# Optimization experiments

Hardware: AMD Instinct MI355X
Metric: run time of the kernel (lower is better)

## Reference

```python
import jax, jax.numpy as jnp
import numpy as np

N = 100000   # nodes
E = 3200000  # edges (avg degree 32)
G = 512      # graphs in batch
IN = 128     # in_channels
H1, C1 = 8, 8  # conv1 heads, per-head channels
OUT = 64     # out_channels (conv2, 1 head)
NEG_SLOPE = 0.2


def setup_inputs() -> dict:
    key = jax.random.key(0)
    ks = jax.random.split(key, 12)
    s = 0.1
    return dict(
        x=jax.random.normal(ks[0], (N, IN), jnp.float32),
        edge_index=jax.random.randint(ks[1], (2, E), 0, N),
        batch=jnp.sort(jax.random.randint(ks[2], (N,), 0, G)),
        W1=jax.random.normal(ks[3], (IN, H1 * C1), jnp.float32) * s,
        att_src1=jax.random.normal(ks[4], (H1, C1), jnp.float32) * s,
        att_dst1=jax.random.normal(ks[5], (H1, C1), jnp.float32) * s,
        b1=jnp.zeros((H1 * C1,), jnp.float32),
        W2=jax.random.normal(ks[6], (H1 * C1, OUT), jnp.float32) * s,
        att_src2=jax.random.normal(ks[7], (1, OUT), jnp.float32) * s,
        att_dst2=jax.random.normal(ks[8], (1, OUT), jnp.float32) * s,
        b2=jnp.zeros((OUT,), jnp.float32),
        lw1=jax.random.normal(ks[9], (OUT, 128), jnp.float32) * s,
        lb1=jnp.zeros((128,), jnp.float32),
        lw2=jax.random.normal(ks[10], (128, 1), jnp.float32) * s,
        lb2=jnp.zeros((1,), jnp.float32),
    )


def gat_layer(x, src, dst, W, a_src, a_dst, bias, heads, outc):
    # PyG GATConv (eval mode): linear -> per-edge leaky_relu attention ->
    # segment softmax over incoming edges per dst -> weighted scatter-add.
    n = x.shape[0]
    h = (x @ W).reshape(n, heads, outc)                      # [N,H,C]
    a_s = jnp.einsum('nhc,hc->nh', h, a_src)                 # [N,H]
    a_d = jnp.einsum('nhc,hc->nh', h, a_dst)
    e = jax.nn.leaky_relu(a_s[src] + a_d[dst], NEG_SLOPE)    # [E',H]
    m = jax.ops.segment_max(e, dst, num_segments=n)
    m = jax.lax.stop_gradient(jnp.where(jnp.isfinite(m), m, 0.0))
    ex = jnp.exp(e - m[dst])
    denom = jax.ops.segment_sum(ex, dst, num_segments=n)
    alpha = ex / jnp.maximum(denom[dst], 1e-16)              # [E',H]
    out = jax.ops.segment_sum(h[src] * alpha[:, :, None], dst, num_segments=n)
    return out.reshape(n, heads * outc) + bias


def reference(x, W1, att_src1, att_dst1, b1, W2, att_src2, att_dst2, b2,
              lw1, lb1, lw2, lb2, edge_index, batch):
    n = x.shape[0]
    loops = jnp.arange(n)                                    # add_self_loops=True
    src = jnp.concatenate([edge_index[0], loops])
    dst = jnp.concatenate([edge_index[1], loops])
    h = jax.nn.elu(gat_layer(x, src, dst, W1, att_src1, att_dst1, b1, H1, C1))
    h = gat_layer(h, src, dst, W2, att_src2, att_dst2, b2, 1, OUT)  # [N,OUT]
    # global_mean_pool
    s = jax.ops.segment_sum(h, batch, num_segments=G)
    cnt = jax.ops.segment_sum(jnp.ones((n, 1), h.dtype), batch, num_segments=G)
    g = s / jnp.maximum(cnt, 1.0)                            # [G,OUT]
    g = jax.nn.elu(g @ lw1 + lb1)
    return g @ lw2 + lb2                                     # [G,1]
```

## Files before the change

### kernel.cpp

```cpp
#include <hip/hip_runtime.h>
#include <hip/hip_fp16.h>
#include <math.h>

#define NN   100000
#define EE   3200000
#define GG   512
#define INC  128
#define D1   64
#define OUTC 64
#define HID  128
#define NEG  0.2f

#define BINS 391
#define BCAP 9216
#define BKBLK 1563

typedef __attribute__((ext_vector_type(2))) float v2f;

__global__ __launch_bounds__(256)
void k_fused(const int* __restrict__ srcv, const int* __restrict__ dstv,
             int* __restrict__ cursor, int* __restrict__ bucket,
             const float* __restrict__ x, const float* __restrict__ W1,
             const float* __restrict__ att_s, const float* __restrict__ att_d,
             unsigned int* __restrict__ h1, __half* __restrict__ a_s,
             float* __restrict__ a_d) {
    __shared__ __align__(16) char smem[45824];
    int tid = threadIdx.x;
    if (blockIdx.x < BKBLK) {
        int* hcnt  = (int*)smem;
        int* hbase = hcnt + BINS;
        for (int i = tid; i < BINS; i += 256) hcnt[i] = 0;
        __syncthreads();
        int e0 = blockIdx.x * 2048;
        int bn[8], rk[8], pk[8];
#pragma unroll
        for (int q = 0; q < 8; ++q) {
            int e = e0 + q * 256 + tid;
            if (e < EE) {
                int s = srcv[e], d = dstv[e];
                bn[q] = d >> 8;
                pk[q] = (s << 8) | (d & 255);
                rk[q] = atomicAdd(&hcnt[bn[q]], 1);
            } else bn[q] = -1;
        }
        __syncthreads();
        for (int i = tid; i < BINS; i += 256) {
            int c = hcnt[i];
            hbase[i] = c ? atomicAdd(&cursor[i], c) : 0;
        }
        __syncthreads();
#pragma unroll
        for (int q = 0; q < 8; ++q) {
            if (bn[q] >= 0) {
                int p = hbase[bn[q]] + rk[q];
                if (p < BCAP) bucket[bn[q] * BCAP + p] = pk[q];
            }
        }
    } else {
        float4* sW4 = (float4*)smem;
        float (*sx)[INC + 4] = (float(*)[INC + 4])(smem + 32768);
        float (*sh)[D1] = (float(*)[D1])(smem + 32768 + 8448);
        float* satt = (float*)(smem + 32768 + 8448 + 4096);
        const float4* W4 = (const float4*)W1;
        for (int i = tid; i < INC * 16; i += 256) sW4[i] = W4[i];
        if (tid < 128) satt[tid] = (tid < 64) ? att_s[tid] : att_d[tid - 64];
        int node0 = (blockIdx.x - BKBLK) * 16;
        for (int i = tid; i < 16 * 32; i += 256) {
            int r = i >> 5, kk = i & 31;
            float4 v = ((const float4*)x)[(node0 + r) * 32 + kk];
            sx[r][kk * 4 + 0] = v.x; sx[r][kk * 4 + 1] = v.y;
            sx[r][kk * 4 + 2] = v.z; sx[r][kk * 4 + 3] = v.w;
        }
        __syncthreads();
        int r = tid >> 4, cg = tid & 15;
        float4 acc = {0.f, 0.f, 0.f, 0.f};
#pragma unroll 8
        for (int k = 0; k < INC; ++k) {
            float xv = sx[r][k];
            float4 wv = sW4[k * 16 + cg];
            acc.x = fmaf(xv, wv.x, acc.x);
            acc.y = fmaf(xv, wv.y, acc.y);
            acc.z = fmaf(xv, wv.z, acc.z);
            acc.w = fmaf(xv, wv.w, acc.w);
        }
        int p = __builtin_amdgcn_cvt_pk_fp8_f32(acc.x, acc.y, 0, false);
        p = __builtin_amdgcn_cvt_pk_fp8_f32(acc.z, acc.w, p, true);
        h1[(node0 + r) * 16 + cg] = (unsigned int)p;
        sh[r][cg * 4 + 0] = acc.x; sh[r][cg * 4 + 1] = acc.y;
        sh[r][cg * 4 + 2] = acc.z; sh[r][cg * 4 + 3] = acc.w;
        __syncthreads();
        if (tid < 128) {
            int rr = tid >> 3, hh = tid & 7;
            float as = 0.f, ad = 0.f;
#pragma unroll
            for (int j = 0; j < 8; ++j) {
                float v = sh[rr][hh * 8 + j];
                as = fmaf(v, satt[hh * 8 + j], as);
                ad = fmaf(v, satt[64 + hh * 8 + j], ad);
            }
            int nb = node0 + rr;
            a_s[nb * 8 + hh] = __float2half(as);
            a_d[nb * 8 + hh] = ad;
        }
    }
}

__global__ __launch_bounds__(256)
void k_binCSR(const int* __restrict__ cursor, const int* __restrict__ bucket,
              int* __restrict__ col, int* __restrict__ rbeg, int* __restrict__ rend) {
    __shared__ int cnt[256];
    __shared__ int tmp[256];
    __shared__ int cur[256];
    int b = blockIdx.x, tid = threadIdx.x;
    cnt[tid] = 0;
    __syncthreads();
    int m = cursor[b]; if (m > BCAP) m = BCAP;
    const int* seg = bucket + b * BCAP;
    for (int i = tid; i < m; i += 256)
        atomicAdd(&cnt[seg[i] & 255], 1);
    __syncthreads();
    tmp[tid] = cnt[tid];
    __syncthreads();
    for (int off = 1; off < 256; off <<= 1) {
        int t = (tid >= off) ? tmp[tid - off] : 0;
        __syncthreads();
        tmp[tid] += t;
        __syncthreads();
    }
    int excl = tmp[tid] - cnt[tid];
    int n = b * 256 + tid;
    if (n < NN) {
        rbeg[n] = b * BCAP + excl;
        rend[n] = b * BCAP + excl + cnt[tid];
    }
    cur[tid] = excl;
    __syncthreads();
    for (int i = tid; i < m; i += 256) {
        int pkv = seg[i];
        int r = atomicAdd(&cur[pkv & 255], 1);
        col[b * BCAP + r] = pkv >> 8;
    }
}

__global__ __launch_bounds__(256, 8)
void k_gat_agg1(const int* __restrict__ rbeg, const int* __restrict__ rend,
                const int* __restrict__ col,
                const __half* __restrict__ a_s, const float* __restrict__ a_d,
                const unsigned int* __restrict__ h1, const float* __restrict__ b1,
                float* __restrict__ out) {
    int wv = threadIdx.x >> 6;
    int lane = threadIdx.x & 63;
    int half = lane >> 5;
    int d = blockIdx.x * 8 + wv * 2 + half;
    int gs = (lane >> 3) & 3;
    int l = lane & 7;
    int rb = rbeg[d], re = rend[d];
    float adh = a_d[d * 8 + l];
    const uint2* hp = (const uint2*)h1;
    uint2 rself = hp[d * 8 + l];
    float asself = __half2float(a_s[d * 8 + l]);
    float ac[8] = {0.f,0.f,0.f,0.f,0.f,0.f,0.f,0.f};
    float denom = 0.f;
    int e = rb + gs;
    int s[4];
#pragma unroll
    for (int q = 0; q < 4; ++q) s[q] = col[e + 4 * q];
    for (; e + 12 < re; ) {
        uint2 rr[4]; float asv[4]; int sn[4];
#pragma unroll
        for (int q = 0; q < 4; ++q) rr[q] = hp[s[q] * 8 + l];
#pragma unroll
        for (int q = 0; q < 4; ++q) asv[q] = __half2float(a_s[s[q] * 8 + l]);
        int en = e + 16;
#pragma unroll
        for (int q = 0; q < 4; ++q) sn[q] = col[en + 4 * q];
#pragma unroll
        for (int q = 0; q < 4; ++q) {
            float xx = asv[q] + adh;
            xx = xx >= 0.f ? xx : NEG * xx;
            float w = __expf(xx);
            denom += w;
            v2f f0 = __builtin_amdgcn_cvt_pk_f32_fp8((int)rr[q].x, false);
            v2f f1 = __builtin_amdgcn_cvt_pk_f32_fp8((int)rr[q].x, true);
            v2f f2 = __builtin_amdgcn_cvt_pk_f32_fp8((int)rr[q].y, false);
            v2f f3 = __builtin_amdgcn_cvt_pk_f32_fp8((int)rr[q].y, true);
            ac[0] = fmaf(f0.x, w, ac[0]); ac[1] = fmaf(f0.y, w, ac[1]);
            ac[2] = fmaf(f1.x, w, ac[2]); ac[3] = fmaf(f1.y, w, ac[3]);
            ac[4] = fmaf(f2.x, w, ac[4]); ac[5] = fmaf(f2.y, w, ac[5]);
            ac[6] = fmaf(f3.x, w, ac[6]); ac[7] = fmaf(f3.y, w, ac[7]);
        }
        e = en;
#pragma unroll
        for (int q = 0; q < 4; ++q) s[q] = sn[q];
    }
    for (; e < re; e += 4) {
        int s0 = col[e];
        uint2 r0 = hp[s0 * 8 + l];
        float x0 = __half2float(a_s[s0 * 8 + l]) + adh;
        x0 = x0 >= 0.f ? x0 : NEG * x0;
        float w0 = __expf(x0);
        denom += w0;
        v2f f0 = __builtin_amdgcn_cvt_pk_f32_fp8((int)r0.x, false);
        v2f f1 = __builtin_amdgcn_cvt_pk_f32_fp8((int)r0.x, true);
        v2f f2 = __builtin_amdgcn_cvt_pk_f32_fp8((int)r0.y, false);
        v2f f3 = __builtin_amdgcn_cvt_pk_f32_fp8((int)r0.y, true);
        ac[0] = fmaf(f0.x, w0, ac[0]); ac[1] = fmaf(f0.y, w0, ac[1]);
        ac[2] = fmaf(f1.x, w0, ac[2]); ac[3] = fmaf(f1.y, w0, ac[3]);
        ac[4] = fmaf(f2.x, w0, ac[4]); ac[5] = fmaf(f2.y, w0, ac[5]);
        ac[6] = fmaf(f3.x, w0, ac[6]); ac[7] = fmaf(f3.y, w0, ac[7]);
    }
    if (gs == 0) {
        float es = asself + adh;
        es = es >= 0.f ? es : NEG * es;
        float w = __expf(es);
        denom += w;
        v2f f0 = __builtin_amdgcn_cvt_pk_f32_fp8((int)rself.x, false);
        v2f f1 = __builtin_amdgcn_cvt_pk_f32_fp8((int)rself.x, true);
        v2f f2 = __builtin_amdgcn_cvt_pk_f32_fp8((int)rself.y, false);
        v2f f3 = __builtin_amdgcn_cvt_pk_f32_fp8((int)rself.y, true);
        ac[0] = fmaf(f0.x, w, ac[0]); ac[1] = fmaf(f0.y, w, ac[1]);
        ac[2] = fmaf(f1.x, w, ac[2]); ac[3] = fmaf(f1.y, w, ac[3]);
        ac[4] = fmaf(f2.x, w, ac[4]); ac[5] = fmaf(f2.y, w, ac[5]);
        ac[6] = fmaf(f3.x, w, ac[6]); ac[7] = fmaf(f3.y, w, ac[7]);
    }
#pragma unroll
    for (int i = 0; i < 8; ++i) {
        ac[i] += __shfl_xor(ac[i], 8, 64);
        ac[i] += __shfl_xor(ac[i], 16, 64);
    }
    denom += __shfl_xor(denom, 8, 64);
    denom += __shfl_xor(denom, 16, 64);
    if (gs == 0) {
        float inv = 1.0f / denom;
        float4 b0 = ((const float4*)b1)[l * 2];
        float4 b4 = ((const float4*)b1)[l * 2 + 1];
        float4 r0, r1;
        r0.x = fmaf(ac[0], inv, b0.x); r0.x = r0.x > 0.f ? r0.x : expm1f(r0.x);
        r0.y = fmaf(ac[1], inv, b0.y); r0.y = r0.y > 0.f ? r0.y : expm1f(r0.y);
        r0.z = fmaf(ac[2], inv, b0.z); r0.z = r0.z > 0.f ? r0.z : expm1f(r0.z);
        r0.w = fmaf(ac[3], inv, b0.w); r0.w = r0.w > 0.f ? r0.w : expm1f(r0.w);
        r1.x = fmaf(ac[4], inv, b4.x); r1.x = r1.x > 0.f ? r1.x : expm1f(r1.x);
        r1.y = fmaf(ac[5], inv, b4.y); r1.y = r1.y > 0.f ? r1.y : expm1f(r1.y);
        r1.z = fmaf(ac[6], inv, b4.z); r1.z = r1.z > 0.f ? r1.z : expm1f(r1.z);
        r1.w = fmaf(ac[7], inv, b4.w); r1.w = r1.w > 0.f ? r1.w : expm1f(r1.w);
        ((float4*)out)[d * 16 + l * 2]     = r0;
        ((float4*)out)[d * 16 + l * 2 + 1] = r1;
    }
}

__global__ __launch_bounds__(256)
void k_lin2(const float* __restrict__ hin, const float* __restrict__ W2,
            const float* __restrict__ att_s, const float* __restrict__ att_d,
            unsigned int* __restrict__ h2, float* __restrict__ a_s,
            float* __restrict__ a_d) {
    __shared__ float4 sW4[D1 * 16];
    __shared__ float sx[16][D1 + 4];
    __shared__ float satt[2 * OUTC];
    int tid = threadIdx.x;
    const float4* W4 = (const float4*)W2;
    for (int i = tid; i < D1 * 16; i += 256) sW4[i] = W4[i];
    if (tid < 128) satt[tid] = (tid < 64) ? att_s[tid] : att_d[tid - 64];
    int node0 = blockIdx.x * 16;
    for (int i = tid; i < 16 * 16; i += 256) {
        int r = i >> 4, kk = i & 15;
        float4 v = ((const float4*)hin)[(node0 + r) * 16 + kk];
        sx[r][kk * 4 + 0] = v.x; sx[r][kk * 4 + 1] = v.y;
        sx[r][kk * 4 + 2] = v.z; sx[r][kk * 4 + 3] = v.w;
    }
    __syncthreads();
    int r = tid >> 4, cg = tid & 15;
    float4 acc = {0.f, 0.f, 0.f, 0.f};
#pragma unroll 8
    for (int k = 0; k < D1; ++k) {
        float xv = sx[r][k];
        float4 wv = sW4[k * 16 + cg];
        acc.x = fmaf(xv, wv.x, acc.x);
        acc.y = fmaf(xv, wv.y, acc.y);
        acc.z = fmaf(xv, wv.z, acc.z);
        acc.w = fmaf(xv, wv.w, acc.w);
    }
    int n = node0 + r;
    int p = __builtin_amdgcn_cvt_pk_fp8_f32(acc.x, acc.y, 0, false);
    p = __builtin_amdgcn_cvt_pk_fp8_f32(acc.z, acc.w, p, true);
    h2[n * 16 + cg] = (unsigned int)p;
    float vs = acc.x * satt[cg * 4] + acc.y * satt[cg * 4 + 1]
             + acc.z * satt[cg * 4 + 2] + acc.w * satt[cg * 4 + 3];
    float vd = acc.x * satt[64 + cg * 4] + acc.y * satt[64 + cg * 4 + 1]
             + acc.z * satt[64 + cg * 4 + 2] + acc.w * satt[64 + cg * 4 + 3];
    for (int off = 1; off < 16; off <<= 1) {
        vs += __shfl_xor(vs, off, 64);
        vd += __shfl_xor(vd, off, 64);
    }
    if (cg == 0) { a_s[n] = vs; a_d[n] = vd; }
}

__global__ __launch_bounds__(256, 8)
void k_gat_agg2(const int* __restrict__ rbeg, const int* __restrict__ rend,
                const int* __restrict__ col,
                const float* __restrict__ a_s, const float* __restrict__ a_d,
                const unsigned int* __restrict__ h2, const float* __restrict__ b2,
                const int* __restrict__ batch,
                float* __restrict__ pool, float* __restrict__ cnt) {
    __shared__ float sv[8][64];
    __shared__ int sgi[8];
    int wv = threadIdx.x >> 6;
    int lane = threadIdx.x & 63;
    int half = lane >> 5;
    int idx = wv * 2 + half;
    int d = blockIdx.x * 8 + idx;
    int gs = (lane >> 3) & 3;
    int l = lane & 7;
    int rb = rbeg[d], re = rend[d];
    float ad = a_d[d];
    const uint2* hp = (const uint2*)h2;
    uint2 rself = hp[d * 8 + l];
    float asself = a_s[d];
    if (gs == 0 && l == 0) sgi[idx] = batch[d];
    float ac[8] = {0.f,0.f,0.f,0.f,0.f,0.f,0.f,0.f};
    float denom = 0.f;
    int e = rb + gs;
    int s[4];
#pragma unroll
    for (int q = 0; q < 4; ++q) s[q] = col[e + 4 * q];
    for (; e + 12 < re; ) {
        uint2 rr[4]; float asv[4]; int sn[4];
#pragma unroll
        for (int q = 0; q < 4; ++q) rr[q] = hp[s[q] * 8 + l];
#pragma unroll
        for (int q = 0; q < 4; ++q) asv[q] = a_s[s[q]];
        int en = e + 16;
#pragma unroll
        for (int q = 0; q < 4; ++q) sn[q] = col[en + 4 * q];
#pragma unroll
        for (int q = 0; q < 4; ++q) {
            float xx = asv[q] + ad;
            xx = xx >= 0.f ? xx : NEG * xx;
            float w = __expf(xx);
            denom += w;
            v2f f0 = __builtin_amdgcn_cvt_pk_f32_fp8((int)rr[q].x, false);
            v2f f1 = __builtin_amdgcn_cvt_pk_f32_fp8((int)rr[q].x, true);
            v2f f2 = __builtin_amdgcn_cvt_pk_f32_fp8((int)rr[q].y, false);
            v2f f3 = __builtin_amdgcn_cvt_pk_f32_fp8((int)rr[q].y, true);
            ac[0] = fmaf(f0.x, w, ac[0]); ac[1] = fmaf(f0.y, w, ac[1]);
            ac[2] = fmaf(f1.x, w, ac[2]); ac[3] = fmaf(f1.y, w, ac[3]);
            ac[4] = fmaf(f2.x, w, ac[4]); ac[5] = fmaf(f2.y, w, ac[5]);
            ac[6] = fmaf(f3.x, w, ac[6]); ac[7] = fmaf(f3.y, w, ac[7]);
        }
        e = en;
#pragma unroll
        for (int q = 0; q < 4; ++q) s[q] = sn[q];
    }
    for (; e < re; e += 4) {
        int s0 = col[e];
        uint2 r0 = hp[s0 * 8 + l];
        float x0 = a_s[s0] + ad;
        x0 = x0 >= 0.f ? x0 : NEG * x0;
        float w0 = __expf(x0);
        denom += w0;
        v2f f0 = __builtin_amdgcn_cvt_pk_f32_fp8((int)r0.x, false);
        v2f f1 = __builtin_amdgcn_cvt_pk_f32_fp8((int)r0.x, true);
        v2f f2 = __builtin_amdgcn_cvt_pk_f32_fp8((int)r0.y, false);
        v2f f3 = __builtin_amdgcn_cvt_pk_f32_fp8((int)r0.y, true);
        ac[0] = fmaf(f0.x, w0, ac[0]); ac[1] = fmaf(f0.y, w0, ac[1]);
        ac[2] = fmaf(f1.x, w0, ac[2]); ac[3] = fmaf(f1.y, w0, ac[3]);
        ac[4] = fmaf(f2.x, w0, ac[4]); ac[5] = fmaf(f2.y, w0, ac[5]);
        ac[6] = fmaf(f3.x, w0, ac[6]); ac[7] = fmaf(f3.y, w0, ac[7]);
    }
    if (gs == 0) {
        float es = asself + ad;
        es = es >= 0.f ? es : NEG * es;
        float w = __expf(es);
        denom += w;
        v2f f0 = __builtin_amdgcn_cvt_pk_f32_fp8((int)rself.x, false);
        v2f f1 = __builtin_amdgcn_cvt_pk_f32_fp8((int)rself.x, true);
        v2f f2 = __builtin_amdgcn_cvt_pk_f32_fp8((int)rself.y, false);
        v2f f3 = __builtin_amdgcn_cvt_pk_f32_fp8((int)rself.y, true);
        ac[0] = fmaf(f0.x, w, ac[0]); ac[1] = fmaf(f0.y, w, ac[1]);
        ac[2] = fmaf(f1.x, w, ac[2]); ac[3] = fmaf(f1.y, w, ac[3]);
        ac[4] = fmaf(f2.x, w, ac[4]); ac[5] = fmaf(f2.y, w, ac[5]);
        ac[6] = fmaf(f3.x, w, ac[6]); ac[7] = fmaf(f3.y, w, ac[7]);
    }
#pragma unroll
    for (int i = 0; i < 8; ++i) {
        ac[i] += __shfl_xor(ac[i], 8, 64);
        ac[i] += __shfl_xor(ac[i], 16, 64);
    }
    denom += __shfl_xor(denom, 8, 64);
    denom += __shfl_xor(denom, 16, 64);
    if (gs == 0) {
        float inv = 1.0f / denom;
#pragma unroll
        for (int i = 0; i < 8; ++i)
            sv[idx][l * 8 + i] = fmaf(ac[i], inv, b2[l * 8 + i]);
    }
    __syncthreads();
    int tid = threadIdx.x;
    if (tid < 64) {
        float acc = sv[0][tid]; int curg = sgi[0];
        for (int r = 1; r < 8; ++r) {
            if (sgi[r] == curg) acc += sv[r][tid];
            else { atomicAdd(&pool[curg * 64 + tid], acc); curg = sgi[r]; acc = sv[r][tid]; }
        }
        atomicAdd(&pool[curg * 64 + tid], acc);
    } else if (tid == 64) {
        float c = 1.f; int curg = sgi[0];
        for (int r = 1; r < 8; ++r) {
            if (sgi[r] == curg) c += 1.f;
            else { atomicAdd(&cnt[curg], c); curg = sgi[r]; c = 1.f; }
        }
        atomicAdd(&cnt[curg], c);
    }
}

__global__ __launch_bounds__(128)
void k_mlp(const float* __restrict__ pool, const float* __restrict__ cnt,
           const float* __restrict__ lw1, const float* __restrict__ lb1,
           const float* __restrict__ lw2, const float* __restrict__ lb2,
           float* __restrict__ out) {
    __shared__ float sg[OUTC];
    __shared__ float sh[HID];
    int g = blockIdx.x, tid = threadIdx.x;
    float c = fmaxf(cnt[g], 1.0f);
    if (tid < OUTC) sg[tid] = pool[g * OUTC + tid] / c;
    __syncthreads();
    float acc = lb1[tid];
#pragma unroll 8
    for (int k = 0; k < OUTC; ++k)
        acc = fmaf(sg[k], lw1[k * HID + tid], acc);
    acc = acc > 0.f ? acc : expm1f(acc);
    sh[tid] = acc * lw2[tid];
    __syncthreads();
    for (int off = 64; off >= 1; off >>= 1) {
        if (tid < off) sh[tid] += sh[tid + off];
        __syncthreads();
    }
    if (tid == 0) out[g] = sh[0] + lb2[0];
}

extern "C" void kernel_launch(void* const* d_in, const int* in_sizes, int n_in,
                              void* d_out, int out_size, void* d_ws, size_t ws_size,
                              hipStream_t stream) {
    const float* x    = (const float*)d_in[0];
    const int*   ei   = (const int*)d_in[1];
    const int*   batch= (const int*)d_in[2];
    const float* W1   = (const float*)d_in[3];
    const float* as1  = (const float*)d_in[4];
    const float* ad1  = (const float*)d_in[5];
    const float* b1   = (const float*)d_in[6];
    const float* W2   = (const float*)d_in[7];
    const float* as2  = (const float*)d_in[8];
    const float* ad2  = (const float*)d_in[9];
    const float* b2   = (const float*)d_in[10];
    const float* lw1  = (const float*)d_in[11];
    const float* lb1  = (const float*)d_in[12];
    const float* lw2  = (const float*)d_in[13];
    const float* lb2  = (const float*)d_in[14];
    float* out = (float*)d_out;

    unsigned int* H8 = (unsigned int*)d_ws;
    float* B    = (float*)(H8 + (size_t)NN * 16);
    float* aD1  = B + (size_t)NN * 64;
    float* aS2  = aD1 + NN * 8;
    float* aD2  = aS2 + NN;
    float* pool = aD2 + NN;
    float* cnt  = pool + GG * 64;
    __half* aS1h = (__half*)(cnt + GG);
    int* rbeg   = (int*)(aS1h + (size_t)NN * 8);
    int* rend   = rbeg + NN;
    int* cursor = rend + NN;
    int* bucket = cursor + BINS;
    int* colv   = bucket + (size_t)BINS * BCAP;

    const int* srcv = ei;
    const int* dstv = ei + EE;

    hipMemsetAsync(cursor, 0, BINS * sizeof(int), stream);
    hipMemsetAsync(pool, 0, (size_t)(GG * 64 + GG) * sizeof(float), stream);

    k_fused<<<BKBLK + NN / 16, 256, 0, stream>>>(srcv, dstv, cursor, bucket,
                                                 x, W1, as1, ad1, H8, aS1h, aD1);
    k_binCSR<<<BINS, 256, 0, stream>>>(cursor, bucket, colv, rbeg, rend);

    k_gat_agg1<<<NN / 8, 256, 0, stream>>>(rbeg, rend, colv, aS1h, aD1, H8, b1, B);

    k_lin2    <<<NN / 16, 256, 0, stream>>>(B, W2, as2, ad2, H8, aS2, aD2);
    k_gat_agg2<<<NN / 8, 256, 0, stream>>>(rbeg, rend, colv, aS2, aD2, H8, b2, batch, pool, cnt);

    k_mlp<<<GG, 128, 0, stream>>>(pool, cnt, lw1, lb1, lw2, lb2, out);
}
```

Before: 386.3 us.

## Register-tile both node linear layers with 256-node blocks and swizzled transposed LDS

```diff
diff --git a/kernel.cpp b/kernel.cpp
--- a/kernel.cpp
+++ b/kernel.cpp
@@ -14,24 +14,102 @@
 #define BINS 391
 #define BCAP 9216
 #define BKBLK 1563
+#define NGB 391
 
 typedef __attribute__((ext_vector_type(2))) float v2f;
 
-__global__ __launch_bounds__(256)
+__global__ __launch_bounds__(256, 3)
 void k_fused(const int* __restrict__ srcv, const int* __restrict__ dstv,
              int* __restrict__ cursor, int* __restrict__ bucket,
              const float* __restrict__ x, const float* __restrict__ W1,
              const float* __restrict__ att_s, const float* __restrict__ att_d,
              unsigned int* __restrict__ h1, __half* __restrict__ a_s,
              float* __restrict__ a_d) {
-    __shared__ __align__(16) char smem[45824];
+    __shared__ __align__(16) char smem[49152];
     int tid = threadIdx.x;
-    if (blockIdx.x < BKBLK) {
+    if (blockIdx.x < NGB) {
+        float4* sW4 = (float4*)smem;
+        float (*sxT)[256] = (float(*)[256])(smem + 32768);
+        const float4* W4 = (const float4*)W1;
+        for (int i = tid; i < 128 * 16; i += 256) sW4[i] = W4[i];
+        int node0 = blockIdx.x * 256;
+        int rg = tid >> 3, cg = tid & 7;
+        float acc[8][8];
+#pragma unroll
+        for (int ii = 0; ii < 8; ++ii)
+#pragma unroll
+            for (int jj = 0; jj < 8; ++jj) acc[ii][jj] = 0.f;
+        const float4* x4 = (const float4*)x;
+        for (int kt = 0; kt < 8; ++kt) {
+            if (kt) __syncthreads();
+#pragma unroll
+            for (int q = 0; q < 4; ++q) {
+                int i = q * 256 + tid;
+                int r = i >> 2, kc = i & 3;
+                int gn = node0 + r;
+                float4 v = {0.f, 0.f, 0.f, 0.f};
+                if (gn < NN) v = x4[(size_t)gn * 32 + kt * 4 + kc];
+                int cs = r ^ (kc << 3);
+                sxT[kc * 4 + 0][cs] = v.x;
+                sxT[kc * 4 + 1][cs] = v.y;
+                sxT[kc * 4 + 2][cs] = v.z;
+                sxT[kc * 4 + 3][cs] = v.w;
+            }
+            __syncthreads();
+#pragma unroll 4
+            for (int kk = 0; kk < 16; ++kk) {
+                int sw = (kk >> 2) << 3;
+                const float* xr = &sxT[kk][(rg * 8) ^ sw];
+                float4 xa = *(const float4*)xr;
+                float4 xb = *(const float4*)(xr + 4);
+                int kg = kt * 16 + kk;
+                float4 wa = sW4[kg * 16 + cg * 2];
+                float4 wb = sW4[kg * 16 + cg * 2 + 1];
+                float xv[8] = {xa.x, xa.y, xa.z, xa.w, xb.x, xb.y, xb.z, xb.w};
+                float wv[8] = {wa.x, wa.y, wa.z, wa.w, wb.x, wb.y, wb.z, wb.w};
+#pragma unroll
+                for (int ii = 0; ii < 8; ++ii)
+#pragma unroll
+                    for (int jj = 0; jj < 8; ++jj)
+                        acc[ii][jj] = fmaf(xv[ii], wv[jj], acc[ii][jj]);
+            }
+        }
+        float4 s0 = ((const float4*)att_s)[cg * 2];
+        float4 s1 = ((const float4*)att_s)[cg * 2 + 1];
+        float4 d0 = ((const float4*)att_d)[cg * 2];
+        float4 d1 = ((const float4*)att_d)[cg * 2 + 1];
+        uint2* hp2 = (uint2*)h1;
+#pragma unroll
+        for (int ii = 0; ii < 8; ++ii) {
+            int n = node0 + rg * 8 + ii;
+            if (n < NN) {
+                float* a = acc[ii];
+                int p0 = __builtin_amdgcn_cvt_pk_fp8_f32(a[0], a[1], 0, false);
+                p0 = __builtin_amdgcn_cvt_pk_fp8_f32(a[2], a[3], p0, true);
+                int p1 = __builtin_amdgcn_cvt_pk_fp8_f32(a[4], a[5], 0, false);
+                p1 = __builtin_amdgcn_cvt_pk_fp8_f32(a[6], a[7], p1, true);
+                uint2 pk; pk.x = (unsigned)p0; pk.y = (unsigned)p1;
+                hp2[n * 8 + cg] = pk;
+                float as = a[0] * s0.x;
+                as = fmaf(a[1], s0.y, as); as = fmaf(a[2], s0.z, as);
+                as = fmaf(a[3], s0.w, as); as = fmaf(a[4], s1.x, as);
+                as = fmaf(a[5], s1.y, as); as = fmaf(a[6], s1.z, as);
+                as = fmaf(a[7], s1.w, as);
+                float ad = a[0] * d0.x;
+                ad = fmaf(a[1], d0.y, ad); ad = fmaf(a[2], d0.z, ad);
+                ad = fmaf(a[3], d0.w, ad); ad = fmaf(a[4], d1.x, ad);
+                ad = fmaf(a[5], d1.y, ad); ad = fmaf(a[6], d1.z, ad);
+                ad = fmaf(a[7], d1.w, ad);
+                a_s[n * 8 + cg] = __float2half(as);
+                a_d[n * 8 + cg] = ad;
+            }
+        }
+    } else {
         int* hcnt  = (int*)smem;
         int* hbase = hcnt + BINS;
         for (int i = tid; i < BINS; i += 256) hcnt[i] = 0;
         __syncthreads();
-        int e0 = blockIdx.x * 2048;
+        int e0 = (blockIdx.x - NGB) * 2048;
         int bn[8], rk[8], pk[8];
 #pragma unroll
         for (int q = 0; q < 8; ++q) {
@@ -55,52 +133,6 @@
                 int p = hbase[bn[q]] + rk[q];
                 if (p < BCAP) bucket[bn[q] * BCAP + p] = pk[q];
             }
-        }
-    } else {
-        float4* sW4 = (float4*)smem;
-        float (*sx)[INC + 4] = (float(*)[INC + 4])(smem + 32768);
-        float (*sh)[D1] = (float(*)[D1])(smem + 32768 + 8448);
-        float* satt = (float*)(smem + 32768 + 8448 + 4096);
-        const float4* W4 = (const float4*)W1;
-        for (int i = tid; i < INC * 16; i += 256) sW4[i] = W4[i];
-        if (tid < 128) satt[tid] = (tid < 64) ? att_s[tid] : att_d[tid - 64];
-        int node0 = (blockIdx.x - BKBLK) * 16;
-        for (int i = tid; i < 16 * 32; i += 256) {
-            int r = i >> 5, kk = i & 31;
-            float4 v = ((const float4*)x)[(node0 + r) * 32 + kk];
-            sx[r][kk * 4 + 0] = v.x; sx[r][kk * 4 + 1] = v.y;
-            sx[r][kk * 4 + 2] = v.z; sx[r][kk * 4 + 3] = v.w;
-        }
-        __syncthreads();
-        int r = tid >> 4, cg = tid & 15;
-        float4 acc = {0.f, 0.f, 0.f, 0.f};
-#pragma unroll 8
-        for (int k = 0; k < INC; ++k) {
-            float xv = sx[r][k];
-            float4 wv = sW4[k * 16 + cg];
-            acc.x = fmaf(xv, wv.x, acc.x);
-            acc.y = fmaf(xv, wv.y, acc.y);
-            acc.z = fmaf(xv, wv.z, acc.z);
-            acc.w = fmaf(xv, wv.w, acc.w);
-        }
-        int p = __builtin_amdgcn_cvt_pk_fp8_f32(acc.x, acc.y, 0, false);
-        p = __builtin_amdgcn_cvt_pk_fp8_f32(acc.z, acc.w, p, true);
-        h1[(node0 + r) * 16 + cg] = (unsigned int)p;
-        sh[r][cg * 4 + 0] = acc.x; sh[r][cg * 4 + 1] = acc.y;
-        sh[r][cg * 4 + 2] = acc.z; sh[r][cg * 4 + 3] = acc.w;
-        __syncthreads();
-        if (tid < 128) {
-            int rr = tid >> 3, hh = tid & 7;
-            float as = 0.f, ad = 0.f;
-#pragma unroll
-            for (int j = 0; j < 8; ++j) {
-                float v = sh[rr][hh * 8 + j];
-                as = fmaf(v, satt[hh * 8 + j], as);
-                ad = fmaf(v, satt[64 + hh * 8 + j], ad);
-            }
-            int nb = node0 + rr;
-            a_s[nb * 8 + hh] = __float2half(as);
-            a_d[nb * 8 + hh] = ad;
         }
     }
 }
@@ -248,50 +280,91 @@
     }
 }
 
-__global__ __launch_bounds__(256)
+__global__ __launch_bounds__(256, 3)
 void k_lin2(const float* __restrict__ hin, const float* __restrict__ W2,
             const float* __restrict__ att_s, const float* __restrict__ att_d,
             unsigned int* __restrict__ h2, float* __restrict__ a_s,
             float* __restrict__ a_d) {
     __shared__ float4 sW4[D1 * 16];
-    __shared__ float sx[16][D1 + 4];
-    __shared__ float satt[2 * OUTC];
+    __shared__ float sxT[32][256];
     int tid = threadIdx.x;
     const float4* W4 = (const float4*)W2;
     for (int i = tid; i < D1 * 16; i += 256) sW4[i] = W4[i];
-    if (tid < 128) satt[tid] = (tid < 64) ? att_s[tid] : att_d[tid - 64];
-    int node0 = blockIdx.x * 16;
-    for (int i = tid; i < 16 * 16; i += 256) {
-        int r = i >> 4, kk = i & 15;
-        float4 v = ((const float4*)hin)[(node0 + r) * 16 + kk];
-        sx[r][kk * 4 + 0] = v.x; sx[r][kk * 4 + 1] = v.y;
-        sx[r][kk * 4 + 2] = v.z; sx[r][kk * 4 + 3] = v.w;
-    }
-    __syncthreads();
-    int r = tid >> 4, cg = tid & 15;
-    float4 acc = {0.f, 0.f, 0.f, 0.f};
-#pragma unroll 8
-    for (int k = 0; k < D1; ++k) {
-        float xv = sx[r][k];
-        float4 wv = sW4[k * 16 + cg];
-        acc.x = fmaf(xv, wv.x, acc.x);
-        acc.y = fmaf(xv, wv.y, acc.y);
-        acc.z = fmaf(xv, wv.z, acc.z);
-        acc.w = fmaf(xv, wv.w, acc.w);
-    }
-    int n = node0 + r;
-    int p = __builtin_amdgcn_cvt_pk_fp8_f32(acc.x, acc.y, 0, false);
-    p = __builtin_amdgcn_cvt_pk_fp8_f32(acc.z, acc.w, p, true);
-    h2[n * 16 + cg] = (unsigned int)p;
-    float vs = acc.x * satt[cg * 4] + acc.y * satt[cg * 4 + 1]
-             + acc.z * satt[cg * 4 + 2] + acc.w * satt[cg * 4 + 3];
-    float vd = acc.x * satt[64 + cg * 4] + acc.y * satt[64 + cg * 4 + 1]
-             + acc.z * satt[64 + cg * 4 + 2] + acc.w * satt[64 + cg * 4 + 3];
-    for (int off = 1; off < 16; off <<= 1) {
-        vs += __shfl_xor(vs, off, 64);
-        vd += __shfl_xor(vd, off, 64);
-    }
-    if (cg == 0) { a_s[n] = vs; a_d[n] = vd; }
+    int node0 = blockIdx.x * 256;
+    int rg = tid >> 3, cg = tid & 7;
+    float acc[8][8];
+#pragma unroll
+    for (int ii = 0; ii < 8; ++ii)
+#pragma unroll
+        for (int jj = 0; jj < 8; ++jj) acc[ii][jj] = 0.f;
+    const float4* x4 = (const float4*)hin;
+    for (int kt = 0; kt < 2; ++kt) {
+        if (kt) __syncthreads();
+#pragma unroll
+        for (int q = 0; q < 8; ++q) {
+            int i = q * 256 + tid;
+            int r = i >> 3, kc = i & 7;
+            int gn = node0 + r;
+            float4 v = {0.f, 0.f, 0.f, 0.f};
+            if (gn < NN) v = x4[(size_t)gn * 16 + kt * 8 + kc];
+            int cs = r ^ (kc << 3);
+            sxT[kc * 4 + 0][cs] = v.x;
+            sxT[kc * 4 + 1][cs] = v.y;
+            sxT[kc * 4 + 2][cs] = v.z;
+            sxT[kc * 4 + 3][cs] = v.w;
+        }
+        __syncthreads();
+#pragma unroll 4
+        for (int kk = 0; kk < 32; ++kk) {
+            int sw = (kk >> 2) << 3;
+            const float* xr = &sxT[kk][(rg * 8) ^ sw];
+            float4 xa = *(const float4*)xr;
+            float4 xb = *(const float4*)(xr + 4);
+            int kg = kt * 32 + kk;
+            float4 wa = sW4[kg * 16 + cg * 2];
+            float4 wb = sW4[kg * 16 + cg * 2 + 1];
+            float xv[8] = {xa.x, xa.y, xa.z, xa.w, xb.x, xb.y, xb.z, xb.w};
+            float wv[8] = {wa.x, wa.y, wa.z, wa.w, wb.x, wb.y, wb.z, wb.w};
+#pragma unroll
+            for (int ii = 0; ii < 8; ++ii)
+#pragma unroll
+                for (int jj = 0; jj < 8; ++jj)
+                    acc[ii][jj] = fmaf(xv[ii], wv[jj], acc[ii][jj]);
+        }
+    }
+    float4 s0 = ((const float4*)att_s)[cg * 2];
+    float4 s1 = ((const float4*)att_s)[cg * 2 + 1];
+    float4 d0 = ((const float4*)att_d)[cg * 2];
+    float4 d1 = ((const float4*)att_d)[cg * 2 + 1];
+    uint2* hp2 = (uint2*)h2;
+#pragma unroll
+    for (int ii = 0; ii < 8; ++ii) {
+        int n = node0 + rg * 8 + ii;
+        if (n < NN) {
+            float* a = acc[ii];
+            int p0 = __builtin_amdgcn_cvt_pk_fp8_f32(a[0], a[1], 0, false);
+            p0 = __builtin_amdgcn_cvt_pk_fp8_f32(a[2], a[3], p0, true);
+            int p1 = __builtin_amdgcn_cvt_pk_fp8_f32(a[4], a[5], 0, false);
+            p1 = __builtin_amdgcn_cvt_pk_fp8_f32(a[6], a[7], p1, true);
+            uint2 pk; pk.x = (unsigned)p0; pk.y = (unsigned)p1;
+            hp2[n * 8 + cg] = pk;
+            float vs = a[0] * s0.x;
+            vs = fmaf(a[1], s0.y, vs); vs = fmaf(a[2], s0.z, vs);
+            vs = fmaf(a[3], s0.w, vs); vs = fmaf(a[4], s1.x, vs);
+            vs = fmaf(a[5], s1.y, vs); vs = fmaf(a[6], s1.z, vs);
+            vs = fmaf(a[7], s1.w, vs);
+            float vd = a[0] * d0.x;
+            vd = fmaf(a[1], d0.y, vd); vd = fmaf(a[2], d0.z, vd);
+            vd = fmaf(a[3], d0.w, vd); vd = fmaf(a[4], d1.x, vd);
+            vd = fmaf(a[5], d1.y, vd); vd = fmaf(a[6], d1.z, vd);
+            vd = fmaf(a[7], d1.w, vd);
+            vs += __shfl_xor(vs, 1, 64); vs += __shfl_xor(vs, 2, 64);
+            vs += __shfl_xor(vs, 4, 64);
+            vd += __shfl_xor(vd, 1, 64); vd += __shfl_xor(vd, 2, 64);
+            vd += __shfl_xor(vd, 4, 64);
+            if (cg == 0) { a_s[n] = vs; a_d[n] = vd; }
+        }
+    }
 }
 
 __global__ __launch_bounds__(256, 8)
@@ -477,13 +550,13 @@
     hipMemsetAsync(cursor, 0, BINS * sizeof(int), stream);
     hipMemsetAsync(pool, 0, (size_t)(GG * 64 + GG) * sizeof(float), stream);
 
-    k_fused<<<BKBLK + NN / 16, 256, 0, stream>>>(srcv, dstv, cursor, bucket,
-                                                 x, W1, as1, ad1, H8, aS1h, aD1);
+    k_fused<<<NGB + BKBLK, 256, 0, stream>>>(srcv, dstv, cursor, bucket,
+                                             x, W1, as1, ad1, H8, aS1h, aD1);
     k_binCSR<<<BINS, 256, 0, stream>>>(cursor, bucket, colv, rbeg, rend);
 
     k_gat_agg1<<<NN / 8, 256, 0, stream>>>(rbeg, rend, colv, aS1h, aD1, H8, b1, B);
 
-    k_lin2    <<<NN / 16, 256, 0, stream>>>(B, W2, as2, ad2, H8, aS2, aD2);
+    k_lin2    <<<NGB, 256, 0, stream>>>(B, W2, as2, ad2, H8, aS2, aD2);
     k_gat_agg2<<<NN / 8, 256, 0, stream>>>(rbeg, rend, colv, aS2, aD2, H8, b2, batch, pool, cnt);
 
     k_mlp<<<GG, 128, 0, stream>>>(pool, cnt, lw1, lb1, lw2, lb2, out);
```

Measured after the change: 353.2 us. 1.09x faster.
